# Kernel optimization log

Measured on AMD Instinct MI355X. Metric: run time of the kernel, lower is better.

Reference implementation:

```python
import jax, jax.numpy as jnp
import numpy as np

HIDDEN = 100
LAYERS = 10
B, T = 512, 512
INIT = 0.1  # 1/sqrt(hidden_size), torch default uniform bound


def setup_inputs() -> dict:
    key = jax.random.key(0)
    ks = jax.random.split(key, 9)
    u = lambda k, shape: jax.random.uniform(k, shape, jnp.float32, -INIT, INIT)
    return {
        "x": jax.random.normal(ks[0], (B, T, 1), jnp.float32),
        "hidden_state": jnp.zeros((LAYERS, B, HIDDEN), jnp.float32),
        "W_ih0": u(ks[1], (HIDDEN, 1)),
        "W_ih": u(ks[2], (LAYERS - 1, HIDDEN, HIDDEN)),
        "W_hh": u(ks[3], (LAYERS, HIDDEN, HIDDEN)),
        "b_ih": u(ks[4], (LAYERS, HIDDEN)),
        "b_hh": u(ks[5], (LAYERS, HIDDEN)),
        "W_out": u(ks[6], (1, HIDDEN)),
        "b_out": u(ks[7], (1,)),
    }


def reference(x, hidden_state, W_ih0, W_ih, W_hh, b_ih, b_hh, W_out, b_out):
    # Multi-layer tanh RNN (batch_first). Scan over time; fixed loop over 10 layers.
    def step(h, x_t):  # h: [L, B, H], x_t: [B, 1]
        inp = x_t
        new_h = []
        for l in range(LAYERS):
            Wi = W_ih0 if l == 0 else W_ih[l - 1]
            hl = jnp.tanh(inp @ Wi.T + b_ih[l] + h[l] @ W_hh[l].T + b_hh[l])
            new_h.append(hl)
            inp = hl
        return jnp.stack(new_h), inp  # carry, top-layer output [B, H]

    h_final, top = jax.lax.scan(step, hidden_state, jnp.swapaxes(x, 0, 1))
    rnn_output = jnp.swapaxes(top, 0, 1)  # [B, T, H]
    # Per-timestep Linear == one batched matmul
    outs = rnn_output @ W_out.T + b_out  # [B, T, 1]
    return outs, h_final
```

## Files before the change

kernel.cpp:

```cpp
#include <hip/hip_runtime.h>


#define HH   100
#define HS   132
#define HSS  136
#define NL   10
#define NPAIR 5
#define NIF   4
#define BBS  512
#define TTS  512
#define NB   32
#define BC   16
#define NT   512
#define SLOTS (BC * 128)

typedef __attribute__((ext_vector_type(8))) short short8;
typedef __attribute__((ext_vector_type(4))) float f32x4;
typedef __attribute__((ext_vector_type(4))) unsigned int u32x4;

__global__ void init_ws_kernel(int* wsi) {
  int i = blockIdx.x * blockDim.x + threadIdx.x;
  if (i < 16384) wsi[i] = 0;
}

__device__ __forceinline__ int flag_idx(int iface, int chunk) {
  return (iface * NB + chunk) * 16;
}

__device__ __forceinline__ void lds_barrier() {
  __asm__ __volatile__("s_waitcnt lgkmcnt(0)\n\ts_barrier" ::: "memory");
}
__device__ __forceinline__ void ctl_barrier() {
  __asm__ __volatile__("s_barrier" ::: "memory");
}

__device__ __forceinline__ float fast_tanh(float v) {
  float e = __expf(2.0f * v);
  return 1.0f - 2.0f * __builtin_amdgcn_rcpf(e + 1.0f);
}

__device__ __forceinline__ unsigned short bf_rtn(float x) {
  return (unsigned short)((__float_as_uint(x) + 0x8000u) >> 16);
}

__global__ __launch_bounds__(NT, 1) void rnn_pipe(
    const float* __restrict__ x,
    const float* __restrict__ h0,
    const float* __restrict__ Wih0,
    const float* __restrict__ Wih,
    const float* __restrict__ Whh,
    const float* __restrict__ bih,
    const float* __restrict__ bhh,
    const float* __restrict__ Wout,
    const float* __restrict__ bout,
    float* __restrict__ out,
    unsigned short* __restrict__ ring,
    int*   __restrict__ wsi,
    int Kv, int RDv)
{
  const int pair  = blockIdx.x / NB;
  const int chunk = blockIdx.x % NB;
  const int tid   = threadIdx.x;
  const int grp   = tid >> 8;
  const int wtid  = tid & 255;
  const int layer = pair * 2 + grp;
  const int Km = Kv - 1, RDm = RDv - 1;
  const int NE = BC * HH;

  const int wave = wtid >> 6, lane = wtid & 63;
  const int quad = lane >> 4, lp = lane & 15;
  const bool is_l9 = (grp == 1 && pair == NPAIR - 1);

  __shared__ unsigned short hbufL[2][BC][HSS];
  __shared__ unsigned short hbufU[2][BC][HSS];
  __shared__ unsigned short ibufL[2][BC][HSS];
  __shared__ float biasS[2][HS];
  __shared__ float wi0s[HS];
  __shared__ float wouts[HS];
  __shared__ float xin[2][BC];

  for (int i = tid; i < 2 * BC * HSS; i += NT) {
    (&hbufL[0][0][0])[i] = 0; (&hbufU[0][0][0])[i] = 0; (&ibufL[0][0][0])[i] = 0;
  }
  for (int i = wtid; i < HS; i += 256) {
    float bv = 0.f;
    if (i < HH) bv = bih[layer * HH + i] + bhh[layer * HH + i];
    else if (i == 100 && layer == NL - 1) bv = bout[0];
    biasS[grp][i] = bv;
    if (grp == 0) wi0s[i]  = (i < HH) ? Wih0[i] : 0.f;
    else          wouts[i] = (i < HH) ? Wout[i] : 0.f;
  }
  if (tid < BC) { xin[0][tid] = 0.f; xin[1][tid] = 0.f; }
  __syncthreads();
  for (int idx = wtid; idx < NE; idx += 256) {
    unsigned short v =
        bf_rtn(h0[((size_t)layer * BBS + chunk * BC + idx / HH) * HH + idx % HH]);
    if (grp == 0) hbufL[0][idx / HH][idx % HH] = v;
    else          hbufU[1][idx / HH][idx % HH] = v;
  }

  short8 Bf[8][2];
  #pragma unroll
  for (int kc = 0; kc < 8; ++kc) {
    #pragma unroll
    for (int ntl = 0; ntl < 2; ++ntl) {
      const int n = wave * 32 + ntl * 16 + lp;
      float wv[8];
      #pragma unroll
      for (int j = 0; j < 8; ++j) {
        const int k = kc * 32 + quad * 8 + j;
        float w = 0.f;
        if (kc < 4) {
          if (k < HH) {
            if (n < HH) w = Whh[(size_t)layer * HH * HH + n * HH + k];
            else if (n == 100 && layer == NL - 1) w = Wout[k];
          }
        } else {
          const int kk = k - 128;
          if (layer > 0 && kk >= 0 && kk < HH && n < HH)
            w = Wih[(size_t)(layer - 1) * HH * HH + n * HH + kk];
        }
        wv[j] = w;
      }
      __attribute__((ext_vector_type(4))) unsigned int p1;
      #pragma unroll
      for (int j2 = 0; j2 < 4; ++j2)
        p1[j2] = (unsigned)bf_rtn(wv[2 * j2]) | ((unsigned)bf_rtn(wv[2 * j2 + 1]) << 16);
      Bf[kc][ntl] = __builtin_bit_cast(short8, p1);
    }
  }

  const bool is_cons = (grp == 0 && pair > 0);
  const bool is_prod = (grp == 1 && pair < NPAIR - 1);
  int* prog_in  = is_cons ? wsi + flag_idx(pair - 1, chunk)        : nullptr;
  int* cons_in  = is_cons ? wsi + 8192 + flag_idx(pair - 1, chunk) : nullptr;
  int* prog_out = is_prod ? wsi + flag_idx(pair, chunk)            : nullptr;
  int* cons_out = is_prod ? wsi + 8192 + flag_idx(pair, chunk)     : nullptr;
  unsigned short* ring_in  = is_cons ? ring + (size_t)((pair - 1) * NB + chunk) * RDv * SLOTS : nullptr;
  unsigned short* ring_out = is_prod ? ring + (size_t)(pair * NB + chunk) * RDv * SLOTS       : nullptr;

  const int jcv[2] = { wave * 32 + lp, wave * 32 + 16 + lp };
  const float br[2]  = { biasS[grp][jcv[0]], biasS[grp][jcv[1]] };
  const float w0r[2] = { wi0s[jcv[0]], wi0s[jcv[1]] };
  const float boutv = bout[0];

  f32x4 hreg[2] = {};
  float px = 0.f;
  const int srow = wtid >> 4, scol = (wtid & 15) * 8;

  if (tid == 0 && is_cons) {
    while (__hip_atomic_load(prog_in, __ATOMIC_RELAXED, __HIP_MEMORY_SCOPE_AGENT) < Kv)
      __builtin_amdgcn_s_sleep(1);
    (void)__hip_atomic_load(prog_in, __ATOMIC_ACQUIRE, __HIP_MEMORY_SCOPE_AGENT);
  }
  ctl_barrier();
  if (is_cons) {
    u32x4 g = *(const u32x4*)(ring_in + wtid * 8);
    *(u32x4*)&ibufL[0][srow][scol] = g;
  }
  if (grp == 0 && pair == 0 && wtid < BC)
    xin[0][wtid] = x[(size_t)(chunk * BC + wtid) * TTS];
  __syncthreads();

  for (int s = 0; s <= TTS; ++s) {
    const int par = s & 1, nxt = par ^ 1;
    const bool active = (grp == 0) ? (s < TTS) : (s >= 1);
    const int t = (grp == 0) ? s : s - 1;
    const bool preb = ((s & Km) == Km) && (s + 1 < TTS);
    const bool upub = (s >= 1) && ((s & Km) == 0);

    if (preb) {
      if (tid == 0 && is_cons) {
        while (__hip_atomic_load(prog_in, __ATOMIC_RELAXED, __HIP_MEMORY_SCOPE_AGENT) < s + 1 + Kv)
          __builtin_amdgcn_s_sleep(1);
        (void)__hip_atomic_load(prog_in, __ATOMIC_ACQUIRE, __HIP_MEMORY_SCOPE_AGENT);
      }
      if (tid == 256 && is_prod && s + 1 + Kv > RDv) {
        while (__hip_atomic_load(cons_out, __ATOMIC_RELAXED, __HIP_MEMORY_SCOPE_AGENT) < s + 1 + Kv - RDv)
          __builtin_amdgcn_s_sleep(1);
      }
      ctl_barrier();
    }

    if (is_prod && s >= 2 && ((s - 1) & Km) != 0) {
      u32x4 v = *(const u32x4*)&hbufU[par][srow][scol];
      *(u32x4*)(ring_out + (size_t)((s - 2) & RDm) * SLOTS + wtid * 8) = v;
    }

    u32x4 pv = {};
    bool pre = false;
    if (is_cons && s + 1 < TTS) {
      pv = *(const u32x4*)(ring_in + (size_t)((s + 1) & RDm) * SLOTS + wtid * 8);
      pre = true;
    }
    if (grp == 0 && pair == 0 && s + 1 < TTS && wtid < BC)
      px = x[(size_t)(chunk * BC + wtid) * TTS + (s + 1)];

    if (active) {
      const unsigned short (*myH)[HSS] = (grp == 0) ? hbufL[par] : hbufU[par];
      const unsigned short (*myI)[HSS] = (grp == 0) ? ibufL[par] : hbufL[par];
      short8 Ah[4], AiS[4];
      #pragma unroll
      for (int kc = 0; kc < 4; ++kc)
        Ah[kc] = *(const short8*)&myH[lp][kc * 32 + quad * 8];
      const bool has_in = (grp == 1) || (pair > 0);
      if (has_in) {
        #pragma unroll
        for (int kc = 0; kc < 4; ++kc)
          AiS[kc] = *(const short8*)&myI[lp][kc * 32 + quad * 8];
      } else {
        #pragma unroll
        for (int kc = 0; kc < 4; ++kc) AiS[kc] = short8{};
      }

      unsigned short (*myHn)[HSS] = (grp == 0) ? hbufL[nxt] : hbufU[nxt];
      #pragma unroll
      for (int ntl = 0; ntl < 2; ++ntl) {
        f32x4 aL = (f32x4){br[ntl], br[ntl], br[ntl], br[ntl]};
        f32x4 aH = {}, cL = {}, cH = {};
        if (has_in) {
          cL = __builtin_amdgcn_mfma_f32_16x16x32_bf16(AiS[0], Bf[4][ntl], cL, 0, 0, 0);
          cH = __builtin_amdgcn_mfma_f32_16x16x32_bf16(AiS[2], Bf[6][ntl], cH, 0, 0, 0);
          cL = __builtin_amdgcn_mfma_f32_16x16x32_bf16(AiS[1], Bf[5][ntl], cL, 0, 0, 0);
          cH = __builtin_amdgcn_mfma_f32_16x16x32_bf16(AiS[3], Bf[7][ntl], cH, 0, 0, 0);
        }
        aL = __builtin_amdgcn_mfma_f32_16x16x32_bf16(Ah[0], Bf[0][ntl], aL, 0, 0, 0);
        aH = __builtin_amdgcn_mfma_f32_16x16x32_bf16(Ah[2], Bf[2][ntl], aH, 0, 0, 0);
        aL = __builtin_amdgcn_mfma_f32_16x16x32_bf16(Ah[1], Bf[1][ntl], aL, 0, 0, 0);
        aH = __builtin_amdgcn_mfma_f32_16x16x32_bf16(Ah[3], Bf[3][ntl], aH, 0, 0, 0);
        f32x4 sum = (aL + aH) + (cL + cH);
        #pragma unroll
        for (int r = 0; r < 4; ++r) {
          const int m = quad * 4 + r;
          float v = sum[r];
          if (layer == 0) v += xin[par][m] * w0r[ntl];
          if (is_l9 && jcv[ntl] == 100) {
            if (s >= 2)
              out[(size_t)(chunk * BC + m) * TTS + (s - 2)] = v;
          } else {
            float h = fast_tanh(v);
            hreg[ntl][r] = h;
            if (jcv[ntl] < HH) myHn[m][jcv[ntl]] = bf_rtn(h);
          }
        }
      }

      if (t == TTS - 1) {
        #pragma unroll
        for (int ntl = 0; ntl < 2; ++ntl)
          if (jcv[ntl] < HH)
            #pragma unroll
            for (int r = 0; r < 4; ++r)
              out[(size_t)BBS * TTS +
                  ((size_t)layer * BBS + chunk * BC + quad * 4 + r) * HH + jcv[ntl]] =
                  hreg[ntl][r];
      }
    }

    if (pre) *(u32x4*)&ibufL[nxt][srow][scol] = pv;
    if (grp == 0 && pair == 0 && s + 1 < TTS && wtid < BC) xin[nxt][wtid] = px;

    if (upub) {
      lds_barrier();
      if (is_prod) {
        u32x4 v = *(const u32x4*)&hbufU[nxt][srow][scol];
        *(u32x4*)(ring_out + (size_t)((s - 1) & RDm) * SLOTS + wtid * 8) = v;
      }
      __syncthreads();
      if (tid == 256 && is_prod)
        __hip_atomic_store(prog_out, s, __ATOMIC_RELEASE, __HIP_MEMORY_SCOPE_AGENT);
      if (tid == 0 && is_cons)
        __hip_atomic_store(cons_in, s, __ATOMIC_RELAXED, __HIP_MEMORY_SCOPE_AGENT);
    } else {
      lds_barrier();
    }
  }

  if (is_l9) {
    const int b = wtid >> 4, seg = wtid & 15;
    float sacc = 0.f;
    #pragma unroll
    for (int jj = 0; jj < 7; ++jj) {
      const int j = seg * 7 + jj;
      if (j < HH) {
        float h = __uint_as_float((unsigned)hbufU[1][b][j] << 16);
        sacc += h * wouts[j];
      }
    }
    sacc += __shfl_xor(sacc, 1, 16);
    sacc += __shfl_xor(sacc, 2, 16);
    sacc += __shfl_xor(sacc, 4, 16);
    sacc += __shfl_xor(sacc, 8, 16);
    if ((wtid & 15) == 0)
      out[(size_t)(chunk * BC + b) * TTS + (TTS - 1)] = sacc + boutv;
  }
}

extern "C" void kernel_launch(void* const* d_in, const int* in_sizes, int n_in,
                              void* d_out, int out_size, void* d_ws, size_t ws_size,
                              hipStream_t stream) {
  const float* x    = (const float*)d_in[0];
  const float* h0   = (const float*)d_in[1];
  const float* Wih0 = (const float*)d_in[2];
  const float* Wih  = (const float*)d_in[3];
  const float* Whh  = (const float*)d_in[4];
  const float* bih  = (const float*)d_in[5];
  const float* bhh  = (const float*)d_in[6];
  const float* Wout = (const float*)d_in[7];
  const float* bout = (const float*)d_in[8];
  float* out = (float*)d_out;

  int* wsi = (int*)d_ws;
  unsigned short* ring = (unsigned short*)((char*)d_ws + 65536);

  const size_t slot_bytes = (size_t)SLOTS * 2;
  int RDv = 32;
  while (RDv > 2 && 65536 + (size_t)NIF * NB * RDv * slot_bytes > ws_size)
    RDv >>= 1;
  int Kv = RDv / 4;
  if (Kv < 1) Kv = 1;

  hipLaunchKernelGGL(init_ws_kernel, dim3(64), dim3(256), 0, stream, wsi);
  hipLaunchKernelGGL(rnn_pipe, dim3(NPAIR * NB), dim3(NT), 0, stream,
                     x, h0, Wih0, Wih, Whh, bih, bhh, Wout, bout, out, ring, wsi,
                     Kv, RDv);
}
```

Before: 936.0 us.

## Double threads per block so each wave computes one 16-column output tile

Raises the block size from 512 to 1024 threads, giving each layer group 8 waves instead of 4. Each wave now owns a single 16-wide column tile instead of two, so the per-step MFMA chain per wave is halved and the weight fragments held in registers shrink from 16 to 8. Ring copies and the final reduction are limited to the first 256 threads of each group. This shortens the serial per-timestep critical path, at the cost of more waves taking part in every barrier and more scheduling pressure per CU.

```diff
diff --git a/kernel.cpp b/kernel.cpp
--- a/kernel.cpp
+++ b/kernel.cpp
@@ -11,7 +11,7 @@
 #define TTS  512
 #define NB   32
 #define BC   16
-#define NT   512
+#define NT   1024
 #define SLOTS (BC * 128)
 
 typedef __attribute__((ext_vector_type(8))) short short8;
@@ -61,14 +61,16 @@
   const int pair  = blockIdx.x / NB;
   const int chunk = blockIdx.x % NB;
   const int tid   = threadIdx.x;
-  const int grp   = tid >> 8;
-  const int wtid  = tid & 255;
+  const int grp   = tid >> 9;
+  const int wtid  = tid & 511;
   const int layer = pair * 2 + grp;
   const int Km = Kv - 1, RDm = RDv - 1;
   const int NE = BC * HH;
 
-  const int wave = wtid >> 6, lane = wtid & 63;
+  const int wave = wtid >> 6;
+  const int lane = wtid & 63;
   const int quad = lane >> 4, lp = lane & 15;
+  const int jc   = wave * 16 + lp;
   const bool is_l9 = (grp == 1 && pair == NPAIR - 1);
 
   __shared__ unsigned short hbufL[2][BC][HSS];
@@ -82,7 +84,7 @@
   for (int i = tid; i < 2 * BC * HSS; i += NT) {
     (&hbufL[0][0][0])[i] = 0; (&hbufU[0][0][0])[i] = 0; (&ibufL[0][0][0])[i] = 0;
   }
-  for (int i = wtid; i < HS; i += 256) {
+  for (int i = wtid; i < HS; i += 512) {
     float bv = 0.f;
     if (i < HH) bv = bih[layer * HH + i] + bhh[layer * HH + i];
     else if (i == 100 && layer == NL - 1) bv = bout[0];
@@ -92,42 +94,39 @@
   }
   if (tid < BC) { xin[0][tid] = 0.f; xin[1][tid] = 0.f; }
   __syncthreads();
-  for (int idx = wtid; idx < NE; idx += 256) {
+  for (int idx = wtid; idx < NE; idx += 512) {
     unsigned short v =
         bf_rtn(h0[((size_t)layer * BBS + chunk * BC + idx / HH) * HH + idx % HH]);
     if (grp == 0) hbufL[0][idx / HH][idx % HH] = v;
     else          hbufU[1][idx / HH][idx % HH] = v;
   }
 
-  short8 Bf[8][2];
+  short8 Bf[8];
   #pragma unroll
   for (int kc = 0; kc < 8; ++kc) {
+    const int n = jc;
+    float wv[8];
     #pragma unroll
-    for (int ntl = 0; ntl < 2; ++ntl) {
-      const int n = wave * 32 + ntl * 16 + lp;
-      float wv[8];
-      #pragma unroll
-      for (int j = 0; j < 8; ++j) {
-        const int k = kc * 32 + quad * 8 + j;
-        float w = 0.f;
-        if (kc < 4) {
-          if (k < HH) {
-            if (n < HH) w = Whh[(size_t)layer * HH * HH + n * HH + k];
-            else if (n == 100 && layer == NL - 1) w = Wout[k];
-          }
-        } else {
-          const int kk = k - 128;
-          if (layer > 0 && kk >= 0 && kk < HH && n < HH)
-            w = Wih[(size_t)(layer - 1) * HH * HH + n * HH + kk];
+    for (int j = 0; j < 8; ++j) {
+      const int k = kc * 32 + quad * 8 + j;
+      float w = 0.f;
+      if (kc < 4) {
+        if (k < HH) {
+          if (n < HH) w = Whh[(size_t)layer * HH * HH + n * HH + k];
+          else if (n == 100 && layer == NL - 1) w = Wout[k];
         }
-        wv[j] = w;
-      }
-      __attribute__((ext_vector_type(4))) unsigned int p1;
-      #pragma unroll
-      for (int j2 = 0; j2 < 4; ++j2)
-        p1[j2] = (unsigned)bf_rtn(wv[2 * j2]) | ((unsigned)bf_rtn(wv[2 * j2 + 1]) << 16);
-      Bf[kc][ntl] = __builtin_bit_cast(short8, p1);
-    }
+      } else {
+        const int kk = k - 128;
+        if (layer > 0 && kk >= 0 && kk < HH && n < HH)
+          w = Wih[(size_t)(layer - 1) * HH * HH + n * HH + kk];
+      }
+      wv[j] = w;
+    }
+    __attribute__((ext_vector_type(4))) unsigned int p1;
+    #pragma unroll
+    for (int j2 = 0; j2 < 4; ++j2)
+      p1[j2] = (unsigned)bf_rtn(wv[2 * j2]) | ((unsigned)bf_rtn(wv[2 * j2 + 1]) << 16);
+    Bf[kc] = __builtin_bit_cast(short8, p1);
   }
 
   const bool is_cons = (grp == 0 && pair > 0);
@@ -139,12 +138,11 @@
   unsigned short* ring_in  = is_cons ? ring + (size_t)((pair - 1) * NB + chunk) * RDv * SLOTS : nullptr;
   unsigned short* ring_out = is_prod ? ring + (size_t)(pair * NB + chunk) * RDv * SLOTS       : nullptr;
 
-  const int jcv[2] = { wave * 32 + lp, wave * 32 + 16 + lp };
-  const float br[2]  = { biasS[grp][jcv[0]], biasS[grp][jcv[1]] };
-  const float w0r[2] = { wi0s[jcv[0]], wi0s[jcv[1]] };
+  const float br  = biasS[grp][jc];
+  const float w0r = wi0s[jc];
   const float boutv = bout[0];
 
-  f32x4 hreg[2] = {};
+  f32x4 hreg = {};
   float px = 0.f;
   const int srow = wtid >> 4, scol = (wtid & 15) * 8;
 
@@ -154,7 +152,7 @@
     (void)__hip_atomic_load(prog_in, __ATOMIC_ACQUIRE, __HIP_MEMORY_SCOPE_AGENT);
   }
   ctl_barrier();
-  if (is_cons) {
+  if (is_cons && wtid < 256) {
     u32x4 g = *(const u32x4*)(ring_in + wtid * 8);
     *(u32x4*)&ibufL[0][srow][scol] = g;
   }
@@ -175,21 +173,21 @@
           __builtin_amdgcn_s_sleep(1);
         (void)__hip_atomic_load(prog_in, __ATOMIC_ACQUIRE, __HIP_MEMORY_SCOPE_AGENT);
       }
-      if (tid == 256 && is_prod && s + 1 + Kv > RDv) {
+      if (tid == 512 && is_prod && s + 1 + Kv > RDv) {
         while (__hip_atomic_load(cons_out, __ATOMIC_RELAXED, __HIP_MEMORY_SCOPE_AGENT) < s + 1 + Kv - RDv)
           __builtin_amdgcn_s_sleep(1);
       }
       ctl_barrier();
     }
 
-    if (is_prod && s >= 2 && ((s - 1) & Km) != 0) {
+    if (is_prod && wtid < 256 && s >= 2 && ((s - 1) & Km) != 0) {
       u32x4 v = *(const u32x4*)&hbufU[par][srow][scol];
       *(u32x4*)(ring_out + (size_t)((s - 2) & RDm) * SLOTS + wtid * 8) = v;
     }
 
     u32x4 pv = {};
     bool pre = false;
-    if (is_cons && s + 1 < TTS) {
+    if (is_cons && wtid < 256 && s + 1 < TTS) {
       pv = *(const u32x4*)(ring_in + (size_t)((s + 1) & RDm) * SLOTS + wtid * 8);
       pre = true;
     }
@@ -213,47 +211,40 @@
         for (int kc = 0; kc < 4; ++kc) AiS[kc] = short8{};
       }
 
+      f32x4 a1 = (f32x4){br, br, br, br};
+      f32x4 c1 = {};
+      if (has_in) {
+        #pragma unroll
+        for (int kc = 0; kc < 4; ++kc)
+          c1 = __builtin_amdgcn_mfma_f32_16x16x32_bf16(AiS[kc], Bf[kc + 4], c1, 0, 0, 0);
+      }
+      #pragma unroll
+      for (int kc = 0; kc < 4; ++kc)
+        a1 = __builtin_amdgcn_mfma_f32_16x16x32_bf16(Ah[kc], Bf[kc], a1, 0, 0, 0);
+
       unsigned short (*myHn)[HSS] = (grp == 0) ? hbufL[nxt] : hbufU[nxt];
+      f32x4 sum = a1 + c1;
       #pragma unroll
-      for (int ntl = 0; ntl < 2; ++ntl) {
-        f32x4 aL = (f32x4){br[ntl], br[ntl], br[ntl], br[ntl]};
-        f32x4 aH = {}, cL = {}, cH = {};
-        if (has_in) {
-          cL = __builtin_amdgcn_mfma_f32_16x16x32_bf16(AiS[0], Bf[4][ntl], cL, 0, 0, 0);
-          cH = __builtin_amdgcn_mfma_f32_16x16x32_bf16(AiS[2], Bf[6][ntl], cH, 0, 0, 0);
-          cL = __builtin_amdgcn_mfma_f32_16x16x32_bf16(AiS[1], Bf[5][ntl], cL, 0, 0, 0);
-          cH = __builtin_amdgcn_mfma_f32_16x16x32_bf16(AiS[3], Bf[7][ntl], cH, 0, 0, 0);
+      for (int r = 0; r < 4; ++r) {
+        const int m = quad * 4 + r;
+        float v = sum[r];
+        if (layer == 0) v += xin[par][m] * w0r;
+        if (is_l9 && jc == 100) {
+          if (s >= 2)
+            out[(size_t)(chunk * BC + m) * TTS + (s - 2)] = v;
+        } else {
+          float h = fast_tanh(v);
+          hreg[r] = h;
+          if (jc < HH) myHn[m][jc] = bf_rtn(h);
         }
-        aL = __builtin_amdgcn_mfma_f32_16x16x32_bf16(Ah[0], Bf[0][ntl], aL, 0, 0, 0);
-        aH = __builtin_amdgcn_mfma_f32_16x16x32_bf16(Ah[2], Bf[2][ntl], aH, 0, 0, 0);
-        aL = __builtin_amdgcn_mfma_f32_16x16x32_bf16(Ah[1], Bf[1][ntl], aL, 0, 0, 0);
-        aH = __builtin_amdgcn_mfma_f32_16x16x32_bf16(Ah[3], Bf[3][ntl], aH, 0, 0, 0);
-        f32x4 sum = (aL + aH) + (cL + cH);
+      }
+
+      if (t == TTS - 1 && jc < HH) {
         #pragma unroll
-        for (int r = 0; r < 4; ++r) {
-          const int m = quad * 4 + r;
-          float v = sum[r];
-          if (layer == 0) v += xin[par][m] * w0r[ntl];
-          if (is_l9 && jcv[ntl] == 100) {
-            if (s >= 2)
-              out[(size_t)(chunk * BC + m) * TTS + (s - 2)] = v;
-          } else {
-            float h = fast_tanh(v);
-            hreg[ntl][r] = h;
-            if (jcv[ntl] < HH) myHn[m][jcv[ntl]] = bf_rtn(h);
-          }
-        }
-      }
-
-      if (t == TTS - 1) {
-        #pragma unroll
-        for (int ntl = 0; ntl < 2; ++ntl)
-          if (jcv[ntl] < HH)
-            #pragma unroll
-            for (int r = 0; r < 4; ++r)
-              out[(size_t)BBS * TTS +
-                  ((size_t)layer * BBS + chunk * BC + quad * 4 + r) * HH + jcv[ntl]] =
-                  hreg[ntl][r];
+        for (int r = 0; r < 4; ++r)
+          out[(size_t)BBS * TTS +
+              ((size_t)layer * BBS + chunk * BC + quad * 4 + r) * HH + jc] =
+              hreg[r];
       }
     }
 
@@ -262,12 +253,12 @@
 
     if (upub) {
       lds_barrier();
-      if (is_prod) {
+      if (is_prod && wtid < 256) {
         u32x4 v = *(const u32x4*)&hbufU[nxt][srow][scol];
         *(u32x4*)(ring_out + (size_t)((s - 1) & RDm) * SLOTS + wtid * 8) = v;
       }
       __syncthreads();
-      if (tid == 256 && is_prod)
+      if (tid == 512 && is_prod)
         __hip_atomic_store(prog_out, s, __ATOMIC_RELEASE, __HIP_MEMORY_SCOPE_AGENT);
       if (tid == 0 && is_cons)
         __hip_atomic_store(cons_in, s, __ATOMIC_RELAXED, __HIP_MEMORY_SCOPE_AGENT);
@@ -276,7 +267,7 @@
     }
   }
 
-  if (is_l9) {
+  if (is_l9 && wtid < 256) {
     const int b = wtid >> 4, seg = wtid & 15;
     float sacc = 0.f;
     #pragma unroll
```

Measured after the change: 894.6 us. 1.05x faster.
